# Kernel tuning notes

Hardware: AMD Instinct MI355X
Metric: run time of the kernel (lower is better)

Reference implementation:

```python
import jax, jax.numpy as jnp
import numpy as np

H = 4                      # attention heads
N_A, N_P = 20000, 30000    # author / paper node counts
E = 200000                 # edges per edge type
IN, HID, OUT = 256, 256, 128
NEG_SLOPE = 0.2


def setup_inputs() -> dict:
    key = jax.random.key(0)
    ks = jax.random.split(key, 24)

    def w(k, shape, fan_in):
        return jax.random.normal(k, shape, jnp.float32) / np.float32(np.sqrt(fan_in))

    inp = {
        'x_author': jax.random.normal(ks[0], (N_A, IN), jnp.float32),
        'x_paper':  jax.random.normal(ks[1], (N_P, IN), jnp.float32),
        'src_ap': jax.random.randint(ks[2], (E,), 0, N_A, jnp.int32),
        'dst_ap': jax.random.randint(ks[3], (E,), 0, N_P, jnp.int32),
        'src_pa': jax.random.randint(ks[4], (E,), 0, N_P, jnp.int32),
        'dst_pa': jax.random.randint(ks[5], (E,), 0, N_A, jnp.int32),
        'src_pp': jax.random.randint(ks[6], (E,), 0, N_P, jnp.int32),
        'dst_pp': jax.random.randint(ks[7], (E,), 0, N_P, jnp.int32),
        'src_aa': jax.random.randint(ks[8], (E,), 0, N_A, jnp.int32),
        'dst_aa': jax.random.randint(ks[9], (E,), 0, N_A, jnp.int32),
        # layer 1 params
        'W1_a': w(ks[10], (IN, HID), IN), 'b1_a': jnp.zeros((HID,), jnp.float32),
        'W1_p': w(ks[11], (IN, HID), IN), 'b1_p': jnp.zeros((HID,), jnp.float32),
        'att1_src': w(ks[12], (4, H, HID // H), HID // H),
        'att1_dst': w(ks[13], (4, H, HID // H), HID // H),
        'q1': w(ks[14], (HID,), HID),
        'k1_W': w(ks[15], (HID, HID), HID), 'k1_b': jnp.zeros((HID,), jnp.float32),
        # layer 2 params
        'W2_a': w(ks[16], (HID, OUT), HID), 'b2_a': jnp.zeros((OUT,), jnp.float32),
        'W2_p': w(ks[17], (HID, OUT), HID), 'b2_p': jnp.zeros((OUT,), jnp.float32),
        'att2_src': w(ks[18], (4, H, OUT // H), OUT // H),
        'att2_dst': w(ks[19], (4, H, OUT // H), OUT // H),
        'q2': w(ks[20], (OUT,), OUT),
        'k2_W': w(ks[21], (OUT, OUT), OUT), 'k2_b': jnp.zeros((OUT,), jnp.float32),
    }
    return inp


def _han_layer(h, edges, att_src, att_dst, q, kW, kb, sizes):
    """One HANConv layer. h: dict node_type -> [N, H, D]."""
    outs = {nt: [] for nt in h}
    for i, (st, dt, row, col) in enumerate(edges):
        xs, xd = h[st], h[dt]
        nd = sizes[dt]
        # per-edge additive attention logits  [E, H]
        a = jax.nn.leaky_relu((xs * att_src[i]).sum(-1)[row]
                              + (xd * att_dst[i]).sum(-1)[col], NEG_SLOPE)
        # softmax over incoming edges of each dst node (segment softmax)
        amax = jax.ops.segment_max(a, col, num_segments=nd)
        ea = jnp.exp(a - amax[col])
        denom = jax.ops.segment_sum(ea, col, num_segments=nd)
        alpha = ea / (denom[col] + 1e-16)
        # weighted scatter-sum of source features  [Nd, H, D]
        agg = jax.ops.segment_sum(xs[row] * alpha[:, :, None], col, num_segments=nd)
        outs[dt].append(jax.nn.relu(agg.reshape(nd, -1)))
    # semantic (metapath-level) attention: PyG group()
    res = {}
    for nt, lst in outs.items():
        stk = jnp.stack(lst)  # [M, N, F]
        score = (q * jnp.tanh(stk @ kW + kb).mean(axis=1)).sum(-1)  # [M]
        attn = jax.nn.softmax(score, axis=0)
        res[nt] = jnp.einsum('m,mnf->nf', attn, stk)
    return res


def reference(x_author, x_paper, src_ap, dst_ap, src_pa, dst_pa, src_pp, dst_pp,
              src_aa, dst_aa, W1_a, b1_a, W1_p, b1_p, att1_src, att1_dst, q1,
              k1_W, k1_b, W2_a, b2_a, W2_p, b2_p, att2_src, att2_dst, q2,
              k2_W, k2_b):
    sizes = {'author': N_A, 'paper': N_P}
    edges = [('author', 'paper', src_ap, dst_ap),
             ('paper', 'author', src_pa, dst_pa),
             ('paper', 'paper', src_pp, dst_pp),
             ('author', 'author', src_aa, dst_aa)]
    d1 = W1_a.shape[1] // H
    h1 = {'author': (x_author @ W1_a + b1_a).reshape(N_A, H, d1),
          'paper':  (x_paper @ W1_p + b1_p).reshape(N_P, H, d1)}
    x1 = _han_layer(h1, edges, att1_src, att1_dst, q1, k1_W, k1_b, sizes)
    d2 = W2_a.shape[1] // H
    h2 = {'author': (x1['author'] @ W2_a + b2_a).reshape(N_A, H, d2),
          'paper':  (x1['paper'] @ W2_p + b2_p).reshape(N_P, H, d2)}
    x2 = _han_layer(h2, edges, att2_src, att2_dst, q2, k2_W, k2_b, sizes)
    return x2['author']
```

## Files before the change

### kernel.cpp

```cpp
#include <hip/hip_runtime.h>
#include <math.h>


#define NA 20000
#define NP 30000
#define NE 200000
#define D1 256
#define D2 128

typedef __attribute__((ext_vector_type(8))) short short8v;
typedef __attribute__((ext_vector_type(4))) float floatx4;
typedef __attribute__((ext_vector_type(8))) unsigned short ushort8v;
typedef __attribute__((ext_vector_type(4))) unsigned short ushort4v;

static __device__ __forceinline__ float lrelu(float x) { return x >= 0.f ? x : 0.2f * x; }

static __device__ __forceinline__ unsigned short bftrunc(float x) {
    return (unsigned short)(__float_as_uint(x) >> 16);
}
static __device__ __forceinline__ float bf2f(unsigned short b) {
    return __uint_as_float(((unsigned)b) << 16);
}
static __device__ __forceinline__ unsigned short bfrn(float x) {
    unsigned u = __float_as_uint(x);
    return (unsigned short)((u + 0x7FFFu + ((u >> 16) & 1u)) >> 16);
}

typedef __attribute__((address_space(1))) const unsigned int as1_uint;
typedef __attribute__((address_space(3))) unsigned int as3_uint;
static __device__ __forceinline__ void gl_lds16(const void* g, void* l) {
    __builtin_amdgcn_global_load_lds((as1_uint*)g, (as3_uint*)l, 16, 0, 0);
}

static inline int cdiv(int a, int b) { return (a + b - 1) / b; }

struct CsrBatch {
    const int* srcv[4];
    const int* dstv[4];
    int* cnt[4];
    int* csrc[4];
    int* cdst[4];
};

__global__ __launch_bounds__(256) void count_deg_b(CsrBatch c, int n) {
    const int ty = blockIdx.y;
    const int i = blockIdx.x * 256 + threadIdx.x;
    if (i < n) atomicAdd(&c.cnt[ty][c.dstv[ty][i]], 1);
}

__global__ __launch_bounds__(256) void fill_csr_b(CsrBatch c, int n) {
    const int ty = blockIdx.y;
    const int i = blockIdx.x * 256 + threadIdx.x;
    if (i < n) {
        const int d = c.dstv[ty][i];
        const int p = atomicAdd(&c.cnt[ty][d], 1);
        c.csrc[ty][p] = c.srcv[ty][i];
        c.cdst[ty][p] = d;
    }
}

__global__ __launch_bounds__(1024) void exscan4(int* __restrict__ curbase,
                                                int* __restrict__ rpbase) {
    const int off_c[4] = {0, NP, NP + NA, NP + NA + NP};
    const int off_r[4] = {0, NP + 1, NP + NA + 2, NP + NA + NP + 3};
    const int ns[4] = {NP, NA, NP, NA};
    const int b = blockIdx.x;
    int* cur = curbase + off_c[b];
    int* rp = rpbase + off_r[b];
    const int n = ns[b];
    __shared__ int wsum[16];
    __shared__ int carry_s;
    const int t = threadIdx.x, wv = t >> 6, ln = t & 63;
    if (t == 0) carry_s = 0;
    __syncthreads();
    for (int base = 0; base < n; base += 1024) {
        const int i = base + t;
        const int v = (i < n) ? cur[i] : 0;
        int x = v;
#pragma unroll
        for (int off = 1; off < 64; off <<= 1) {
            int y = __shfl_up(x, off);
            if (ln >= off) x += y;
        }
        if (ln == 63) wsum[wv] = x;
        __syncthreads();
        if (wv == 0) {
            int s = (ln < 16) ? wsum[ln] : 0;
#pragma unroll
            for (int off = 1; off < 16; off <<= 1) {
                int y = __shfl_up(s, off);
                if (ln >= off) s += y;
            }
            if (ln < 16) wsum[ln] = s;
        }
        __syncthreads();
        const int woff = (wv == 0) ? 0 : wsum[wv - 1];
        const int c = carry_s;
        const int ex = c + woff + x - v;
        if (i < n) { rp[i] = ex; cur[i] = ex; }
        __syncthreads();
        if (t == 1023) carry_s = c + wsum[15];
        __syncthreads();
    }
    if (t == 0) rp[n] = carry_s;
}

struct PrepBatch {
    const float* W[6];
    unsigned short* img[6];
    int N[6];
    int nsl[6];
};

__global__ __launch_bounds__(256) void w_prep(PrepBatch p) {
    const int m = blockIdx.y;
    const int idx = blockIdx.x * 256 + threadIdx.x;
    if (idx >= p.nsl[m]) return;
    const int N = p.N[m];
    const int slot = idx & 3;
    const int col = (idx >> 2) % N;
    const int rest = (idx >> 2) / N;
    const int part = rest & 1;
    const int kt = rest >> 1;
    const int ks = slot ^ ((col >> 1) & 3);
    unsigned short* dst = p.img[m] + (((size_t)(kt * 2 + part) * N + col) * 32) + slot * 8;
    const float* wsrc = p.W[m] + (size_t)(kt * 32 + ks * 8) * N + col;
    short8v o;
#pragma unroll
    for (int k = 0; k < 8; ++k) {
        const float x = wsrc[(size_t)k * N];
        const unsigned short hb = bftrunc(x);
        o[k] = part ? (short)bftrunc(x - bf2f(hb)) : (short)hb;
    }
    *(short8v*)dst = o;
}

struct XrBatch {
    const float* x[2];
    unsigned short* o[2];
    int n8[2];
};

__global__ __launch_bounds__(256) void xround_b(XrBatch p) {
    const int m = blockIdx.y;
    const int i = blockIdx.x * 256 + threadIdx.x;
    if (i >= p.n8[m]) return;
    const float* xp = p.x[m] + (size_t)i * 8;
    float4 v0 = *(const float4*)xp;
    float4 v1 = *(const float4*)(xp + 4);
    const float xs8[8] = {v0.x, v0.y, v0.z, v0.w, v1.x, v1.y, v1.z, v1.w};
    short8v o;
#pragma unroll
    for (int k = 0; k < 8; ++k) o[k] = (short)bfrn(xs8[k]);
    *(short8v*)&p.o[m][(size_t)i * 8] = o;
}

template <int NT>
struct GemmBatch {
    const unsigned short* A[NT];
    const unsigned short* Wimg[NT];
    const float* bias[NT];
    unsigned short* C[NT];
    int M[NT];
};

template <int BN, bool SCORE, bool SPLITW, int NT>
__global__ __launch_bounds__(256) void gemm_sw(
    GemmBatch<NT> g, const float* __restrict__ qv, float* __restrict__ score, int K) {
    constexpr int WGN = BN / 64;
    constexpr int WGM = 4 / WGN;
    constexpr int BM = WGM * 64;
    constexpr int NB = SPLITW ? 2 : 1;
    constexpr int ACH = BM * 32 * 2 / 1024;
    constexpr int BCH = NB * BN * 32 * 2 / 1024;
    constexpr int CPW = (ACH + BCH) / 4;
    constexpr int ASZ = BM * 64;
    constexpr int BSZ = NB * BN * 64;
    const int ty = blockIdx.y;
    const int M = g.M[ty];
    const int bm = blockIdx.x * BM;
    if (bm >= M) return;
    const unsigned short* __restrict__ A = g.A[ty];
    const unsigned short* __restrict__ Wi = g.Wimg[ty];
    const float* __restrict__ bias = g.bias[ty];
    __shared__ __attribute__((aligned(16))) unsigned short As[2][BM][32];
    __shared__ __attribute__((aligned(16))) unsigned short Bs[2][NB][BN][32];
    __shared__ float red[256];
    const int t = threadIdx.x;
    const int lane = t & 63, wid = t >> 6;
    const int wr = wid / WGN, wc = wid % WGN;
    const int fq = lane >> 4, fr = lane & 15;
    const int asl = (fq ^ ((fr >> 1) & 3)) * 16;
    const int lr = lane >> 2;
    const int lks = (lane & 3) ^ ((lane >> 3) & 3);
    floatx4 acc[4][4];
#pragma unroll
    for (int i = 0; i < 4; ++i)
#pragma unroll
        for (int j = 0; j < 4; ++j) acc[i][j] = {0.f, 0.f, 0.f, 0.f};

    const int NK = K >> 5;
    auto STAGE = [&](int b, int ki) {
        const char* wbase = (const char*)Wi + (size_t)ki * (2 * BN * 64);
#pragma unroll
        for (int ci = 0; ci < CPW; ++ci) {
            const int c = wid * CPW + ci;
            if (c < ACH) {
                const int row = c * 16 + lr;
                const char* srcp = (const char*)(A + (size_t)(bm + row) * K + ki * 32 + lks * 8);
                gl_lds16(srcp, (char*)As + b * ASZ + c * 1024);
            } else {
                const int bc = c - ACH;
                gl_lds16(wbase + (size_t)bc * 1024 + lane * 16, (char*)Bs + b * BSZ + bc * 1024);
            }
        }
    };
    STAGE(0, 0);
    __syncthreads();
    int cur = 0;
    for (int ki = 0; ki < NK; ++ki) {
        if (ki + 1 < NK) STAGE(cur ^ 1, ki + 1);
        short8v a[4], bh[4], bl[4];
#pragma unroll
        for (int f = 0; f < 4; ++f) {
            const int ar = wr * 64 + f * 16 + fr;
            a[f] = *(const short8v*)((const char*)As + cur * ASZ + ar * 64 + asl);
            const int bc = wc * 64 + f * 16 + fr;
            bh[f] = *(const short8v*)((const char*)Bs + cur * BSZ + bc * 64 + asl);
            if constexpr (SPLITW)
                bl[f] = *(const short8v*)((const char*)Bs + cur * BSZ + (size_t)BN * 64 + bc * 64 + asl);
        }
#pragma unroll
        for (int i = 0; i < 4; ++i)
#pragma unroll
            for (int j = 0; j < 4; ++j) {
                acc[i][j] = __builtin_amdgcn_mfma_f32_16x16x32_bf16(a[i], bh[j], acc[i][j], 0, 0, 0);
                if constexpr (SPLITW)
                    acc[i][j] = __builtin_amdgcn_mfma_f32_16x16x32_bf16(a[i], bl[j], acc[i][j], 0, 0, 0);
            }
        __syncthreads();
        cur ^= 1;
    }
    if constexpr (!SCORE) {
        unsigned short* __restrict__ Cb = g.C[ty];
#pragma unroll
        for (int i = 0; i < 4; ++i) {
            const int gr0 = bm + wr * 64 + i * 16 + fq * 4;
#pragma unroll
            for (int j = 0; j < 4; ++j) {
                const int col = wc * 64 + j * 16 + fr;
                const float b = bias[col];
#pragma unroll
                for (int r = 0; r < 4; ++r) {
                    const int gr = gr0 + r;
                    if (gr < M) Cb[(size_t)gr * BN + col] = bfrn(acc[i][j][r] + b);
                }
            }
        }
    } else {
        float partial = 0.f;
#pragma unroll
        for (int i = 0; i < 4; ++i) {
            const int gr0 = bm + wr * 64 + i * 16 + fq * 4;
#pragma unroll
            for (int j = 0; j < 4; ++j) {
                const int col = wc * 64 + j * 16 + fr;
                const float b = bias[col], q = qv[col];
#pragma unroll
                for (int r = 0; r < 4; ++r) {
                    if (gr0 + r < M) partial += tanhf(acc[i][j][r] + b) * q;
                }
            }
        }
        red[t] = partial;
        __syncthreads();
        for (int s = 128; s > 0; s >>= 1) {
            if (t < s) red[t] += red[t + s];
            __syncthreads();
        }
        if (t == 0) atomicAdd(&score[ty], red[0]);
    }
}

template <int HD, int NSC>
__global__ __launch_bounds__(256) void node_scoresN(
    const unsigned short* __restrict__ hx,
    const float* __restrict__ a0, const float* __restrict__ a1,
    const float* __restrict__ a2, const float* __restrict__ a3,
    float* __restrict__ o0, float* __restrict__ o1,
    float* __restrict__ o2, float* __restrict__ o3, int n) {
    const int idx = blockIdx.x * blockDim.x + threadIdx.x;
    const int node = idx >> 2, hh = idx & 3;
    if (node >= n) return;
    const unsigned short* row = hx + (size_t)node * (4 * HD) + hh * HD;
    float s0 = 0.f, s1 = 0.f, s2 = 0.f, s3 = 0.f;
#pragma unroll
    for (int d = 0; d < HD; d += 4) {
        ushort4v xv = *(const ushort4v*)&row[d];
        const float x0 = bf2f(xv[0]), x1 = bf2f(xv[1]), x2 = bf2f(xv[2]), x3 = bf2f(xv[3]);
        float4 v = *(const float4*)&a0[hh * HD + d];
        s0 += x0 * v.x + x1 * v.y + x2 * v.z + x3 * v.w;
        if constexpr (NSC > 1) {
            v = *(const float4*)&a1[hh * HD + d];
            s1 += x0 * v.x + x1 * v.y + x2 * v.z + x3 * v.w;
        }
        if constexpr (NSC > 2) {
            v = *(const float4*)&a2[hh * HD + d];
            s2 += x0 * v.x + x1 * v.y + x2 * v.z + x3 * v.w;
        }
        if constexpr (NSC > 3) {
            v = *(const float4*)&a3[hh * HD + d];
            s3 += x0 * v.x + x1 * v.y + x2 * v.z + x3 * v.w;
        }
    }
    o0[idx] = s0;
    if constexpr (NSC > 1) o1[idx] = s1;
    if constexpr (NSC > 2) o2[idx] = s2;
    if constexpr (NSC > 3) o3[idx] = s3;
}

template <int NT>
struct ElogBatch {
    const int* csrc[NT];
    const int* cdst[NT];
    const float* ss[NT];
    const float* sd[NT];
    float4* alog[NT];
};

template <int NT>
__global__ __launch_bounds__(256) void edge_logits_b(ElogBatch<NT> a, int n) {
    const int ty = blockIdx.y;
    const int i = blockIdx.x * 256 + threadIdx.x;
    if (i >= n) return;
    const int s = a.csrc[ty][i], d = a.cdst[ty][i];
    const float4 av = *(const float4*)&a.ss[ty][s * 4];
    const float4 bv = *(const float4*)&a.sd[ty][d * 4];
    float4 o = {lrelu(av.x + bv.x), lrelu(av.y + bv.y), lrelu(av.z + bv.z), lrelu(av.w + bv.w)};
    a.alog[ty][i] = o;
}

template <int EPL>
static __device__ __forceinline__ void accum(const unsigned short* p, float ea, float* acc) {
#pragma unroll
    for (int w = 0; w < EPL / 8; ++w) {
        ushort8v x = *(const ushort8v*)(p + w * 8);
#pragma unroll
        for (int k = 0; k < 8; ++k) acc[w * 8 + k] += bf2f(x[k]) * ea;
    }
}

template <int NT>
struct AggBatch {
    const unsigned short* xs[NT];
    const float* alog[NT];
    const int* csrc[NT];
    const int* rowptr[NT];
    unsigned short* out[NT];
    int ndst[NT];
};

template <int D, int NT>
__global__ __launch_bounds__(256) void agg_b(AggBatch<NT> a) {
    constexpr int EPL = D / 16;
    const int ty = blockIdx.y;
    const int gid = blockIdx.x * 16 + (threadIdx.x >> 4);
    if (gid >= a.ndst[ty]) return;
    const int g = threadIdx.x & 15;
    const int h = g >> 2, sub = g & 3;
    const int* __restrict__ rp = a.rowptr[ty];
    const int e0 = rp[gid], e1 = rp[gid + 1];
    const float* __restrict__ lg = a.alog[ty];
    const int* __restrict__ cs = a.csrc[ty];
    const unsigned short* __restrict__ xs = a.xs[ty];
    float mx = -INFINITY;
    for (int e = e0 + sub; e < e1; e += 4)
        mx = fmaxf(mx, lg[(size_t)e * 4 + h]);
    mx = fmaxf(mx, __shfl_xor(mx, 1));
    mx = fmaxf(mx, __shfl_xor(mx, 2));
    float acc[EPL] = {};
    float denom = 0.f;
    int e = e0;
    for (; e + 2 <= e1; e += 2) {
        const int r0 = cs[e], r1 = cs[e + 1];
        const float l0 = lg[(size_t)e * 4 + h];
        const float l1 = lg[(size_t)(e + 1) * 4 + h];
        const float ea0 = __expf(l0 - mx), ea1 = __expf(l1 - mx);
        denom += ea0 + ea1;
        accum<EPL>(xs + (size_t)r0 * D + g * EPL, ea0, acc);
        accum<EPL>(xs + (size_t)r1 * D + g * EPL, ea1, acc);
    }
    if (e < e1) {
        const int r0 = cs[e];
        const float l0 = lg[(size_t)e * 4 + h];
        const float ea0 = __expf(l0 - mx);
        denom += ea0;
        accum<EPL>(xs + (size_t)r0 * D + g * EPL, ea0, acc);
    }
    const float inv = 1.f / (denom + 1e-16f);
    unsigned short* __restrict__ orow = a.out[ty] + (size_t)gid * D + g * EPL;
#pragma unroll
    for (int w = 0; w < EPL / 8; ++w) {
        short8v o;
#pragma unroll
        for (int k = 0; k < 8; ++k)
            o[k] = (short)bfrn(fmaxf(acc[w * 8 + k] * inv, 0.f));
        *(short8v*)&orow[w * 8] = o;
    }
}

struct CombBatch {
    const unsigned short* a[2];
    const unsigned short* b[2];
    unsigned short* o[2];
    int n8[2];
    int slot[2];
    float invN[2];
};

__global__ __launch_bounds__(256) void combine_b(CombBatch c, const float* __restrict__ sc) {
    const int ty = blockIdx.y;
    const int i = blockIdx.x * 256 + threadIdx.x;
    if (i >= c.n8[ty]) return;
    const float s0 = sc[c.slot[ty]] * c.invN[ty];
    const float s1 = sc[c.slot[ty] + 1] * c.invN[ty];
    const float m = fmaxf(s0, s1);
    const float e0 = expf(s0 - m), e1 = expf(s1 - m);
    const float w0 = e0 / (e0 + e1), w1 = e1 / (e0 + e1);
    const size_t o = (size_t)i * 8;
    ushort8v x = *(const ushort8v*)&c.a[ty][o];
    ushort8v y = *(const ushort8v*)&c.b[ty][o];
    short8v r;
#pragma unroll
    for (int k = 0; k < 8; ++k)
        r[k] = (short)bfrn(w0 * bf2f(x[k]) + w1 * bf2f(y[k]));
    *(short8v*)&c.o[ty][o] = r;
}

__global__ __launch_bounds__(256) void combine_out(
    const unsigned short* __restrict__ a, const unsigned short* __restrict__ b,
    float* __restrict__ out, const float* __restrict__ sc, int slot, float invN, int n8) {
    const int i = blockIdx.x * 256 + threadIdx.x;
    if (i >= n8) return;
    const float s0 = sc[slot] * invN, s1 = sc[slot + 1] * invN;
    const float m = fmaxf(s0, s1);
    const float e0 = expf(s0 - m), e1 = expf(s1 - m);
    const float w0 = e0 / (e0 + e1), w1 = e1 / (e0 + e1);
    const size_t o = (size_t)i * 8;
    ushort8v x = *(const ushort8v*)&a[o];
    ushort8v y = *(const ushort8v*)&b[o];
    float rr[8];
#pragma unroll
    for (int k = 0; k < 8; ++k) rr[k] = w0 * bf2f(x[k]) + w1 * bf2f(y[k]);
    float4 r0 = {rr[0], rr[1], rr[2], rr[3]};
    float4 r1 = {rr[4], rr[5], rr[6], rr[7]};
    *(float4*)&out[o] = r0;
    *(float4*)&out[o + 4] = r1;
}

extern "C" void kernel_launch(void* const* d_in, const int* in_sizes, int n_in,
                              void* d_out, int out_size, void* d_ws, size_t ws_size,
                              hipStream_t stream) {
    const float* x_a = (const float*)d_in[0];
    const float* x_p = (const float*)d_in[1];
    const int* src[4] = {(const int*)d_in[2], (const int*)d_in[4], (const int*)d_in[6], (const int*)d_in[8]};
    const int* dst[4] = {(const int*)d_in[3], (const int*)d_in[5], (const int*)d_in[7], (const int*)d_in[9]};
    const float* W1a = (const float*)d_in[10]; const float* b1a = (const float*)d_in[11];
    const float* W1p = (const float*)d_in[12]; const float* b1p = (const float*)d_in[13];
    const float* att1s = (const float*)d_in[14]; const float* att1d = (const float*)d_in[15];
    const float* q1 = (const float*)d_in[16];
    const float* k1W = (const float*)d_in[17]; const float* k1b = (const float*)d_in[18];
    const float* W2a = (const float*)d_in[19]; const float* b2a = (const float*)d_in[20];
    const float* W2p = (const float*)d_in[21]; const float* b2p = (const float*)d_in[22];
    const float* att2s = (const float*)d_in[23]; const float* att2d = (const float*)d_in[24];
    const float* q2 = (const float*)d_in[25];
    const float* k2W = (const float*)d_in[26]; const float* k2b = (const float*)d_in[27];

    const int NAp = NA + 128, NPp = NP + 128;
    char* wp = (char*)d_ws;
    unsigned short* xa_bf = (unsigned short*)wp; wp += (size_t)NAp * D1 * 2;
    unsigned short* xp_bf = (unsigned short*)wp; wp += (size_t)NPp * D1 * 2;
    unsigned short* h1a_bf = (unsigned short*)wp; wp += (size_t)NA * D1 * 2;
    unsigned short* h1p_bf = (unsigned short*)wp; wp += (size_t)NP * D1 * 2;
    unsigned short* a0 = (unsigned short*)wp; wp += (size_t)NPp * D1 * 2;
    unsigned short* a1 = (unsigned short*)wp; wp += (size_t)NAp * D1 * 2;
    unsigned short* a2 = (unsigned short*)wp; wp += (size_t)NPp * D1 * 2;
    unsigned short* a3 = (unsigned short*)wp; wp += (size_t)NAp * D1 * 2;
    float* sv = (float*)wp; wp += (size_t)(16 * NA + 16 * NP) * 4;
    float4* alogb = (float4*)wp; wp += (size_t)4 * NE * 16;
    float* sc = (float*)wp; wp += 16 * 4;
    int* rp_base = (int*)wp; wp += (size_t)(NP + NA + NP + NA + 4) * 4;
    int* cur_base = (int*)wp; wp += (size_t)(NP + NA + NP + NA) * 4;
    int* csrc_base = (int*)wp; wp += (size_t)4 * NE * 4;
    int* cdst_base = (int*)wp; wp += (size_t)4 * NE * 4;
    unsigned short* img_w1a = (unsigned short*)wp; wp += (size_t)8 * 2 * 256 * 32 * 2;
    unsigned short* img_w1p = (unsigned short*)wp; wp += (size_t)8 * 2 * 256 * 32 * 2;
    unsigned short* img_k1w = (unsigned short*)wp; wp += (size_t)8 * 2 * 256 * 32 * 2;
    unsigned short* img_w2a = (unsigned short*)wp; wp += (size_t)8 * 2 * 128 * 32 * 2;
    unsigned short* img_w2p = (unsigned short*)wp; wp += (size_t)8 * 2 * 128 * 32 * 2;
    unsigned short* img_k2w = (unsigned short*)wp; wp += (size_t)4 * 2 * 128 * 32 * 2;
    const size_t need_bytes = (size_t)(wp - (char*)d_ws);
    if (ws_size < need_bytes) return;

    int* rp[4] = {rp_base, rp_base + NP + 1, rp_base + NP + NA + 2, rp_base + NP + NA + NP + 3};
    int* cur[4] = {cur_base, cur_base + NP, cur_base + NP + NA, cur_base + NP + NA + NP};
    int* csrc[4]; int* cdst[4]; float4* alog[4];
    for (int i = 0; i < 4; ++i) {
        csrc[i] = csrc_base + (size_t)i * NE;
        cdst[i] = cdst_base + (size_t)i * NE;
        alog[i] = alogb + (size_t)i * NE;
    }
    float* ss0 = sv;             float* sd0 = ss0 + NA * 4;
    float* ss1 = sd0 + NP * 4;   float* sd1 = ss1 + NP * 4;
    float* ss2 = sd1 + NA * 4;   float* sd2 = ss2 + NP * 4;
    float* ss3 = sd2 + NP * 4;   float* sd3 = ss3 + NA * 4;
    unsigned short* res_p = a0;
    unsigned short* res_a = a1;
    unsigned short* h2a_bf = a2;
    unsigned short* h2p_bf = a2 + (size_t)NA * D2;
    unsigned short* g21 = a3;
    unsigned short* g23 = a3 + (size_t)NAp * D2;
    float* ss21 = sv;             float* sd21 = ss21 + NP * 4;
    float* ss23 = sd21 + NA * 4;  float* sd23 = ss23 + NA * 4;

    hipMemsetAsync(cur_base, 0, (size_t)(NP + NA + NP + NA) * sizeof(int), stream);
    hipMemsetAsync(sc, 0, 16 * sizeof(float), stream);
    PrepBatch pb = {{W1a, W1p, k1W, W2a, W2p, k2W},
                    {img_w1a, img_w1p, img_k1w, img_w2a, img_w2p, img_k2w},
                    {256, 256, 256, 128, 128, 128},
                    {8 * 2 * 256 * 4, 8 * 2 * 256 * 4, 8 * 2 * 256 * 4,
                     8 * 2 * 128 * 4, 8 * 2 * 128 * 4, 4 * 2 * 128 * 4}};
    w_prep<<<dim3(cdiv(8 * 2 * 256 * 4, 256), 6), 256, 0, stream>>>(pb);
    XrBatch xb = {{x_a, x_p}, {xa_bf, xp_bf}, {NA * D1 / 8, NP * D1 / 8}};
    xround_b<<<dim3(cdiv(NP * D1 / 8, 256), 2), 256, 0, stream>>>(xb);

    CsrBatch cb;
    for (int i = 0; i < 4; ++i) {
        cb.srcv[i] = src[i]; cb.dstv[i] = dst[i];
        cb.cnt[i] = cur[i]; cb.csrc[i] = csrc[i]; cb.cdst[i] = cdst[i];
    }
    count_deg_b<<<dim3(cdiv(NE, 256), 4), 256, 0, stream>>>(cb, NE);
    exscan4<<<4, 1024, 0, stream>>>(cur_base, rp_base);
    fill_csr_b<<<dim3(cdiv(NE, 256), 4), 256, 0, stream>>>(cb, NE);

    GemmBatch<2> t1 = {{xa_bf, xp_bf}, {img_w1a, img_w1p}, {b1a, b1p}, {h1a_bf, h1p_bf}, {NA, NP}};
    gemm_sw<256, false, true, 2><<<dim3(cdiv(NP, 64), 2), 256, 0, stream>>>(t1, nullptr, nullptr, 256);

    node_scoresN<64, 4><<<cdiv(NA * 4, 256), 256, 0, stream>>>(
        h1a_bf, att1s + 0 * 256, att1d + 1 * 256, att1s + 3 * 256, att1d + 3 * 256,
        ss0, sd1, ss3, sd3, NA);
    node_scoresN<64, 4><<<cdiv(NP * 4, 256), 256, 0, stream>>>(
        h1p_bf, att1d + 0 * 256, att1s + 1 * 256, att1s + 2 * 256, att1d + 2 * 256,
        sd0, ss1, ss2, sd2, NP);

    ElogBatch<4> el1 = {{csrc[0], csrc[1], csrc[2], csrc[3]},
                        {cdst[0], cdst[1], cdst[2], cdst[3]},
                        {ss0, ss1, ss2, ss3}, {sd0, sd1, sd2, sd3},
                        {alog[0], alog[1], alog[2], alog[3]}};
    edge_logits_b<4><<<dim3(cdiv(NE, 256), 4), 256, 0, stream>>>(el1, NE);
    AggBatch<4> ab1 = {{h1a_bf, h1p_bf, h1p_bf, h1a_bf},
                       {(const float*)alog[0], (const float*)alog[1], (const float*)alog[2], (const float*)alog[3]},
                       {csrc[0], csrc[1], csrc[2], csrc[3]},
                       {rp[0], rp[1], rp[2], rp[3]},
                       {a0, a1, a2, a3},
                       {NP, NA, NP, NA}};
    agg_b<256, 4><<<dim3(cdiv(NP, 16), 4), 256, 0, stream>>>(ab1);

    GemmBatch<4> s1 = {{a0, a2, a1, a3},
                       {img_k1w, img_k1w, img_k1w, img_k1w},
                       {k1b, k1b, k1b, k1b},
                       {nullptr, nullptr, nullptr, nullptr},
                       {NP, NP, NA, NA}};
    gemm_sw<256, true, false, 4><<<dim3(cdiv(NP, 64), 4), 256, 0, stream>>>(s1, q1, sc, 256);
    CombBatch c1 = {{a0, a1}, {a2, a3}, {res_p, res_a},
                    {NP * D1 / 8, NA * D1 / 8}, {0, 2}, {1.f / NP, 1.f / NA}};
    combine_b<<<dim3(cdiv(NP * D1 / 8, 256), 2), 256, 0, stream>>>(c1, sc);

    GemmBatch<2> t2 = {{res_a, res_p}, {img_w2a, img_w2p}, {b2a, b2p}, {h2a_bf, h2p_bf}, {NA, NP}};
    gemm_sw<128, false, true, 2><<<dim3(cdiv(NP, 128), 2), 256, 0, stream>>>(t2, nullptr, nullptr, 256);

    node_scoresN<32, 3><<<cdiv(NA * 4, 256), 256, 0, stream>>>(
        h2a_bf, att2d + 1 * 128, att2s + 3 * 128, att2d + 3 * 128, nullptr,
        sd21, ss23, sd23, nullptr, NA);
    node_scoresN<32, 1><<<cdiv(NP * 4, 256), 256, 0, stream>>>(
        h2p_bf, att2s + 1 * 128, nullptr, nullptr, nullptr,
        ss21, nullptr, nullptr, nullptr, NP);
    ElogBatch<2> el2 = {{csrc[1], csrc[3]}, {cdst[1], cdst[3]},
                        {ss21, ss23}, {sd21, sd23}, {alog[1], alog[3]}};
    edge_logits_b<2><<<dim3(cdiv(NE, 256), 2), 256, 0, stream>>>(el2, NE);
    AggBatch<2> ab2 = {{h2p_bf, h2a_bf},
                       {(const float*)alog[1], (const float*)alog[3]},
                       {csrc[1], csrc[3]}, {rp[1], rp[3]},
                       {g21, g23}, {NA, NA}};
    agg_b<128, 2><<<dim3(cdiv(NA, 16), 2), 256, 0, stream>>>(ab2);

    GemmBatch<2> s2 = {{g21, g23}, {img_k2w, img_k2w}, {k2b, k2b}, {nullptr, nullptr}, {NA, NA}};
    gemm_sw<128, true, false, 2><<<dim3(cdiv(NA, 128), 2), 256, 0, stream>>>(s2, q2, sc + 4, 128);
    combine_out<<<cdiv(NA * D2 / 8, 256), 256, 0, stream>>>(
        g21, g23, (float*)d_out, sc, 4, 1.f / NA, NA * D2 / 8);
}
```

Measured before the change: 417.0 us.

## Fuse edge logits into aggregation, batch node-score kernels, retile GEMM to 128 rows

Edge-logit materialisation is removed: the aggregation kernel now computes leaky-ReLU logits from the per-node source and destination scores directly, and it drops the max-subtraction pass. The two node-score launches per layer become one batched launch, and the two memsets are merged into one. The GEMM is retiled to a fixed 128-row block on a 2x2 wave grid, loading B fragments inside the j loop to cut register pressure. Dropping the softmax max-shift risks overflow in exp for large logits, and the retile changes per-block work and occupancy.

```diff
diff --git a/kernel.cpp b/kernel.cpp
--- a/kernel.cpp
+++ b/kernel.cpp
@@ -167,12 +167,13 @@
 template <int BN, bool SCORE, bool SPLITW, int NT>
 __global__ __launch_bounds__(256) void gemm_sw(
     GemmBatch<NT> g, const float* __restrict__ qv, float* __restrict__ score, int K) {
-    constexpr int WGN = BN / 64;
-    constexpr int WGM = 4 / WGN;
-    constexpr int BM = WGM * 64;
+    constexpr int BM = 128;
+    constexpr int WGM = 2, WGN = 2;
+    constexpr int CW = BN / WGN;
+    constexpr int FB = CW / 16;
     constexpr int NB = SPLITW ? 2 : 1;
-    constexpr int ACH = BM * 32 * 2 / 1024;
-    constexpr int BCH = NB * BN * 32 * 2 / 1024;
+    constexpr int ACH = BM * 64 / 1024;
+    constexpr int BCH = NB * BN * 64 / 1024;
     constexpr int CPW = (ACH + BCH) / 4;
     constexpr int ASZ = BM * 64;
     constexpr int BSZ = NB * BN * 64;
@@ -185,7 +186,6 @@
     const float* __restrict__ bias = g.bias[ty];
     __shared__ __attribute__((aligned(16))) unsigned short As[2][BM][32];
     __shared__ __attribute__((aligned(16))) unsigned short Bs[2][NB][BN][32];
-    __shared__ float red[256];
     const int t = threadIdx.x;
     const int lane = t & 63, wid = t >> 6;
     const int wr = wid / WGN, wc = wid % WGN;
@@ -193,11 +193,11 @@
     const int asl = (fq ^ ((fr >> 1) & 3)) * 16;
     const int lr = lane >> 2;
     const int lks = (lane & 3) ^ ((lane >> 3) & 3);
-    floatx4 acc[4][4];
+    floatx4 acc[4][FB];
 #pragma unroll
     for (int i = 0; i < 4; ++i)
 #pragma unroll
-        for (int j = 0; j < 4; ++j) acc[i][j] = {0.f, 0.f, 0.f, 0.f};
+        for (int j = 0; j < FB; ++j) acc[i][j] = {0.f, 0.f, 0.f, 0.f};
 
     const int NK = K >> 5;
     auto STAGE = [&](int b, int ki) {
@@ -220,24 +220,26 @@
     int cur = 0;
     for (int ki = 0; ki < NK; ++ki) {
         if (ki + 1 < NK) STAGE(cur ^ 1, ki + 1);
-        short8v a[4], bh[4], bl[4];
+        short8v afr[4];
 #pragma unroll
         for (int f = 0; f < 4; ++f) {
             const int ar = wr * 64 + f * 16 + fr;
-            a[f] = *(const short8v*)((const char*)As + cur * ASZ + ar * 64 + asl);
-            const int bc = wc * 64 + f * 16 + fr;
-            bh[f] = *(const short8v*)((const char*)Bs + cur * BSZ + bc * 64 + asl);
-            if constexpr (SPLITW)
-                bl[f] = *(const short8v*)((const char*)Bs + cur * BSZ + (size_t)BN * 64 + bc * 64 + asl);
-        }
-#pragma unroll
-        for (int i = 0; i < 4; ++i)
-#pragma unroll
-            for (int j = 0; j < 4; ++j) {
-                acc[i][j] = __builtin_amdgcn_mfma_f32_16x16x32_bf16(a[i], bh[j], acc[i][j], 0, 0, 0);
-                if constexpr (SPLITW)
-                    acc[i][j] = __builtin_amdgcn_mfma_f32_16x16x32_bf16(a[i], bl[j], acc[i][j], 0, 0, 0);
+            afr[f] = *(const short8v*)((const char*)As + cur * ASZ + ar * 64 + asl);
+        }
+#pragma unroll
+        for (int j = 0; j < FB; ++j) {
+            const int bc = wc * CW + j * 16 + fr;
+            short8v bh = *(const short8v*)((const char*)Bs + cur * BSZ + bc * 64 + asl);
+#pragma unroll
+            for (int i = 0; i < 4; ++i)
+                acc[i][j] = __builtin_amdgcn_mfma_f32_16x16x32_bf16(afr[i], bh, acc[i][j], 0, 0, 0);
+            if constexpr (SPLITW) {
+                short8v bl = *(const short8v*)((const char*)Bs + cur * BSZ + (size_t)BN * 64 + bc * 64 + asl);
+#pragma unroll
+                for (int i = 0; i < 4; ++i)
+                    acc[i][j] = __builtin_amdgcn_mfma_f32_16x16x32_bf16(afr[i], bl, acc[i][j], 0, 0, 0);
             }
+        }
         __syncthreads();
         cur ^= 1;
     }
@@ -247,8 +249,8 @@
         for (int i = 0; i < 4; ++i) {
             const int gr0 = bm + wr * 64 + i * 16 + fq * 4;
 #pragma unroll
-            for (int j = 0; j < 4; ++j) {
-                const int col = wc * 64 + j * 16 + fr;
+            for (int j = 0; j < FB; ++j) {
+                const int col = wc * CW + j * 16 + fr;
                 const float b = bias[col];
 #pragma unroll
                 for (int r = 0; r < 4; ++r) {
@@ -258,13 +260,14 @@
             }
         }
     } else {
+        __shared__ float red[256];
         float partial = 0.f;
 #pragma unroll
         for (int i = 0; i < 4; ++i) {
             const int gr0 = bm + wr * 64 + i * 16 + fq * 4;
 #pragma unroll
-            for (int j = 0; j < 4; ++j) {
-                const int col = wc * 64 + j * 16 + fr;
+            for (int j = 0; j < FB; ++j) {
+                const int col = wc * CW + j * 16 + fr;
                 const float b = bias[col], q = qv[col];
 #pragma unroll
                 for (int r = 0; r < 4; ++r) {
@@ -282,62 +285,38 @@
     }
 }
 
-template <int HD, int NSC>
-__global__ __launch_bounds__(256) void node_scoresN(
-    const unsigned short* __restrict__ hx,
-    const float* __restrict__ a0, const float* __restrict__ a1,
-    const float* __restrict__ a2, const float* __restrict__ a3,
-    float* __restrict__ o0, float* __restrict__ o1,
-    float* __restrict__ o2, float* __restrict__ o3, int n) {
-    const int idx = blockIdx.x * blockDim.x + threadIdx.x;
+struct NsBatch {
+    const unsigned short* hx[2];
+    const float* att[2][4];
+    float* out[2][4];
+    int n[2];
+    int nsc[2];
+};
+
+template <int HD>
+__global__ __launch_bounds__(256) void ns_b(NsBatch p) {
+    const int ty = blockIdx.y;
+    const int idx = blockIdx.x * 256 + threadIdx.x;
     const int node = idx >> 2, hh = idx & 3;
-    if (node >= n) return;
-    const unsigned short* row = hx + (size_t)node * (4 * HD) + hh * HD;
-    float s0 = 0.f, s1 = 0.f, s2 = 0.f, s3 = 0.f;
+    if (node >= p.n[ty]) return;
+    const unsigned short* row = p.hx[ty] + (size_t)node * (4 * HD) + hh * HD;
+    const int nsc = p.nsc[ty];
+    float s[4] = {0.f, 0.f, 0.f, 0.f};
 #pragma unroll
     for (int d = 0; d < HD; d += 4) {
         ushort4v xv = *(const ushort4v*)&row[d];
         const float x0 = bf2f(xv[0]), x1 = bf2f(xv[1]), x2 = bf2f(xv[2]), x3 = bf2f(xv[3]);
-        float4 v = *(const float4*)&a0[hh * HD + d];
-        s0 += x0 * v.x + x1 * v.y + x2 * v.z + x3 * v.w;
-        if constexpr (NSC > 1) {
-            v = *(const float4*)&a1[hh * HD + d];
-            s1 += x0 * v.x + x1 * v.y + x2 * v.z + x3 * v.w;
-        }
-        if constexpr (NSC > 2) {
-            v = *(const float4*)&a2[hh * HD + d];
-            s2 += x0 * v.x + x1 * v.y + x2 * v.z + x3 * v.w;
-        }
-        if constexpr (NSC > 3) {
-            v = *(const float4*)&a3[hh * HD + d];
-            s3 += x0 * v.x + x1 * v.y + x2 * v.z + x3 * v.w;
-        }
-    }
-    o0[idx] = s0;
-    if constexpr (NSC > 1) o1[idx] = s1;
-    if constexpr (NSC > 2) o2[idx] = s2;
-    if constexpr (NSC > 3) o3[idx] = s3;
-}
-
-template <int NT>
-struct ElogBatch {
-    const int* csrc[NT];
-    const int* cdst[NT];
-    const float* ss[NT];
-    const float* sd[NT];
-    float4* alog[NT];
-};
-
-template <int NT>
-__global__ __launch_bounds__(256) void edge_logits_b(ElogBatch<NT> a, int n) {
-    const int ty = blockIdx.y;
-    const int i = blockIdx.x * 256 + threadIdx.x;
-    if (i >= n) return;
-    const int s = a.csrc[ty][i], d = a.cdst[ty][i];
-    const float4 av = *(const float4*)&a.ss[ty][s * 4];
-    const float4 bv = *(const float4*)&a.sd[ty][d * 4];
-    float4 o = {lrelu(av.x + bv.x), lrelu(av.y + bv.y), lrelu(av.z + bv.z), lrelu(av.w + bv.w)};
-    a.alog[ty][i] = o;
+#pragma unroll
+        for (int v = 0; v < 4; ++v) {
+            if (v < nsc) {
+                float4 a = *(const float4*)&p.att[ty][v][hh * HD + d];
+                s[v] += x0 * a.x + x1 * a.y + x2 * a.z + x3 * a.w;
+            }
+        }
+    }
+#pragma unroll
+    for (int v = 0; v < 4; ++v)
+        if (v < nsc) p.out[ty][v][idx] = s[v];
 }
 
 template <int EPL>
@@ -353,7 +332,8 @@
 template <int NT>
 struct AggBatch {
     const unsigned short* xs[NT];
-    const float* alog[NT];
+    const float* ss[NT];
+    const float* sd[NT];
     const int* csrc[NT];
     const int* rowptr[NT];
     unsigned short* out[NT];
@@ -367,33 +347,29 @@
     const int gid = blockIdx.x * 16 + (threadIdx.x >> 4);
     if (gid >= a.ndst[ty]) return;
     const int g = threadIdx.x & 15;
-    const int h = g >> 2, sub = g & 3;
+    const int h = g >> 2;
     const int* __restrict__ rp = a.rowptr[ty];
     const int e0 = rp[gid], e1 = rp[gid + 1];
-    const float* __restrict__ lg = a.alog[ty];
+    const float* __restrict__ ss = a.ss[ty];
     const int* __restrict__ cs = a.csrc[ty];
     const unsigned short* __restrict__ xs = a.xs[ty];
-    float mx = -INFINITY;
-    for (int e = e0 + sub; e < e1; e += 4)
-        mx = fmaxf(mx, lg[(size_t)e * 4 + h]);
-    mx = fmaxf(mx, __shfl_xor(mx, 1));
-    mx = fmaxf(mx, __shfl_xor(mx, 2));
+    const float sdh = a.sd[ty][gid * 4 + h];
     float acc[EPL] = {};
     float denom = 0.f;
     int e = e0;
     for (; e + 2 <= e1; e += 2) {
         const int r0 = cs[e], r1 = cs[e + 1];
-        const float l0 = lg[(size_t)e * 4 + h];
-        const float l1 = lg[(size_t)(e + 1) * 4 + h];
-        const float ea0 = __expf(l0 - mx), ea1 = __expf(l1 - mx);
+        const float l0 = lrelu(ss[r0 * 4 + h] + sdh);
+        const float l1 = lrelu(ss[r1 * 4 + h] + sdh);
+        const float ea0 = __expf(l0), ea1 = __expf(l1);
         denom += ea0 + ea1;
         accum<EPL>(xs + (size_t)r0 * D + g * EPL, ea0, acc);
         accum<EPL>(xs + (size_t)r1 * D + g * EPL, ea1, acc);
     }
     if (e < e1) {
         const int r0 = cs[e];
-        const float l0 = lg[(size_t)e * 4 + h];
-        const float ea0 = __expf(l0 - mx);
+        const float l0 = lrelu(ss[r0 * 4 + h] + sdh);
+        const float ea0 = __expf(l0);
         denom += ea0;
         accum<EPL>(xs + (size_t)r0 * D + g * EPL, ea0, acc);
     }
@@ -487,10 +463,9 @@
     unsigned short* a2 = (unsigned short*)wp; wp += (size_t)NPp * D1 * 2;
     unsigned short* a3 = (unsigned short*)wp; wp += (size_t)NAp * D1 * 2;
     float* sv = (float*)wp; wp += (size_t)(16 * NA + 16 * NP) * 4;
-    float4* alogb = (float4*)wp; wp += (size_t)4 * NE * 16;
-    float* sc = (float*)wp; wp += 16 * 4;
     int* rp_base = (int*)wp; wp += (size_t)(NP + NA + NP + NA + 4) * 4;
     int* cur_base = (int*)wp; wp += (size_t)(NP + NA + NP + NA) * 4;
+    float* sc = (float*)wp; wp += 16 * 4;
     int* csrc_base = (int*)wp; wp += (size_t)4 * NE * 4;
     int* cdst_base = (int*)wp; wp += (size_t)4 * NE * 4;
     unsigned short* img_w1a = (unsigned short*)wp; wp += (size_t)8 * 2 * 256 * 32 * 2;
@@ -504,11 +479,10 @@
 
     int* rp[4] = {rp_base, rp_base + NP + 1, rp_base + NP + NA + 2, rp_base + NP + NA + NP + 3};
     int* cur[4] = {cur_base, cur_base + NP, cur_base + NP + NA, cur_base + NP + NA + NP};
-    int* csrc[4]; int* cdst[4]; float4* alog[4];
+    int* csrc[4]; int* cdst[4];
     for (int i = 0; i < 4; ++i) {
         csrc[i] = csrc_base + (size_t)i * NE;
         cdst[i] = cdst_base + (size_t)i * NE;
-        alog[i] = alogb + (size_t)i * NE;
     }
     float* ss0 = sv;             float* sd0 = ss0 + NA * 4;
     float* ss1 = sd0 + NP * 4;   float* sd1 = ss1 + NP * 4;
@@ -523,8 +497,7 @@
     float* ss21 = sv;             float* sd21 = ss21 + NP * 4;
     float* ss23 = sd21 + NA * 4;  float* sd23 = ss23 + NA * 4;
 
-    hipMemsetAsync(cur_base, 0, (size_t)(NP + NA + NP + NA) * sizeof(int), stream);
-    hipMemsetAsync(sc, 0, 16 * sizeof(float), stream);
+    hipMemsetAsync(cur_base, 0, (size_t)(NP + NA + NP + NA) * sizeof(int) + 16 * sizeof(float), stream);
     PrepBatch pb = {{W1a, W1p, k1W, W2a, W2p, k2W},
                     {img_w1a, img_w1p, img_k1w, img_w2a, img_w2p, img_k2w},
                     {256, 256, 256, 128, 128, 128},
@@ -544,22 +517,21 @@
     fill_csr_b<<<dim3(cdiv(NE, 256), 4), 256, 0, stream>>>(cb, NE);
 
     GemmBatch<2> t1 = {{xa_bf, xp_bf}, {img_w1a, img_w1p}, {b1a, b1p}, {h1a_bf, h1p_bf}, {NA, NP}};
-    gemm_sw<256, false, true, 2><<<dim3(cdiv(NP, 64), 2), 256, 0, stream>>>(t1, nullptr, nullptr, 256);
-
-    node_scoresN<64, 4><<<cdiv(NA * 4, 256), 256, 0, stream>>>(
-        h1a_bf, att1s + 0 * 256, att1d + 1 * 256, att1s + 3 * 256, att1d + 3 * 256,
-        ss0, sd1, ss3, sd3, NA);
-    node_scoresN<64, 4><<<cdiv(NP * 4, 256), 256, 0, stream>>>(
-        h1p_bf, att1d + 0 * 256, att1s + 1 * 256, att1s + 2 * 256, att1d + 2 * 256,
-        sd0, ss1, ss2, sd2, NP);
-
-    ElogBatch<4> el1 = {{csrc[0], csrc[1], csrc[2], csrc[3]},
-                        {cdst[0], cdst[1], cdst[2], cdst[3]},
-                        {ss0, ss1, ss2, ss3}, {sd0, sd1, sd2, sd3},
-                        {alog[0], alog[1], alog[2], alog[3]}};
-    edge_logits_b<4><<<dim3(cdiv(NE, 256), 4), 256, 0, stream>>>(el1, NE);
+    gemm_sw<256, false, true, 2><<<dim3(cdiv(NP, 128), 2), 256, 0, stream>>>(t1, nullptr, nullptr, 256);
+
+    NsBatch n1;
+    n1.hx[0] = h1a_bf; n1.hx[1] = h1p_bf;
+    n1.att[0][0] = att1s + 0 * 256; n1.att[0][1] = att1d + 1 * 256;
+    n1.att[0][2] = att1s + 3 * 256; n1.att[0][3] = att1d + 3 * 256;
+    n1.att[1][0] = att1d + 0 * 256; n1.att[1][1] = att1s + 1 * 256;
+    n1.att[1][2] = att1s + 2 * 256; n1.att[1][3] = att1d + 2 * 256;
+    n1.out[0][0] = ss0; n1.out[0][1] = sd1; n1.out[0][2] = ss3; n1.out[0][3] = sd3;
+    n1.out[1][0] = sd0; n1.out[1][1] = ss1; n1.out[1][2] = ss2; n1.out[1][3] = sd2;
+    n1.n[0] = NA; n1.n[1] = NP; n1.nsc[0] = 4; n1.nsc[1] = 4;
+    ns_b<64><<<dim3(cdiv(NP * 4, 256), 2), 256, 0, stream>>>(n1);
+
     AggBatch<4> ab1 = {{h1a_bf, h1p_bf, h1p_bf, h1a_bf},
-                       {(const float*)alog[0], (const float*)alog[1], (const float*)alog[2], (const float*)alog[3]},
+                       {ss0, ss1, ss2, ss3}, {sd0, sd1, sd2, sd3},
                        {csrc[0], csrc[1], csrc[2], csrc[3]},
                        {rp[0], rp[1], rp[2], rp[3]},
                        {a0, a1, a2, a3},
@@ -571,7 +543,7 @@
                        {k1b, k1b, k1b, k1b},
                        {nullptr, nullptr, nullptr, nullptr},
                        {NP, NP, NA, NA}};
-    gemm_sw<256, true, false, 4><<<dim3(cdiv(NP, 64), 4), 256, 0, stream>>>(s1, q1, sc, 256);
+    gemm_sw<256, true, false, 4><<<dim3(cdiv(NP, 128), 4), 256, 0, stream>>>(s1, q1, sc, 256);
     CombBatch c1 = {{a0, a1}, {a2, a3}, {res_p, res_a},
                     {NP * D1 / 8, NA * D1 / 8}, {0, 2}, {1.f / NP, 1.f / NA}};
     combine_b<<<dim3(cdiv(NP * D1 / 8, 256), 2), 256, 0, stream>>>(c1, sc);
@@ -579,17 +551,19 @@
     GemmBatch<2> t2 = {{res_a, res_p}, {img_w2a, img_w2p}, {b2a, b2p}, {h2a_bf, h2p_bf}, {NA, NP}};
     gemm_sw<128, false, true, 2><<<dim3(cdiv(NP, 128), 2), 256, 0, stream>>>(t2, nullptr, nullptr, 256);
 
-    node_scoresN<32, 3><<<cdiv(NA * 4, 256), 256, 0, stream>>>(
-        h2a_bf, att2d + 1 * 128, att2s + 3 * 128, att2d + 3 * 128, nullptr,
-        sd21, ss23, sd23, nullptr, NA);
-    node_scoresN<32, 1><<<cdiv(NP * 4, 256), 256, 0, stream>>>(
-        h2p_bf, att2s + 1 * 128, nullptr, nullptr, nullptr,
-        ss21, nullptr, nullptr, nullptr, NP);
-    ElogBatch<2> el2 = {{csrc[1], csrc[3]}, {cdst[1], cdst[3]},
-                        {ss21, ss23}, {sd21, sd23}, {alog[1], alog[3]}};
-    edge_logits_b<2><<<dim3(cdiv(NE, 256), 2), 256, 0, stream>>>(el2, NE);
+    NsBatch n2;
+    n2.hx[0] = h2a_bf; n2.hx[1] = h2p_bf;
+    n2.att[0][0] = att2d + 1 * 128; n2.att[0][1] = att2s + 3 * 128;
+    n2.att[0][2] = att2d + 3 * 128; n2.att[0][3] = nullptr;
+    n2.att[1][0] = att2s + 1 * 128; n2.att[1][1] = nullptr;
+    n2.att[1][2] = nullptr; n2.att[1][3] = nullptr;
+    n2.out[0][0] = sd21; n2.out[0][1] = ss23; n2.out[0][2] = sd23; n2.out[0][3] = nullptr;
+    n2.out[1][0] = ss21; n2.out[1][1] = nullptr; n2.out[1][2] = nullptr; n2.out[1][3] = nullptr;
+    n2.n[0] = NA; n2.n[1] = NP; n2.nsc[0] = 3; n2.nsc[1] = 1;
+    ns_b<32><<<dim3(cdiv(NP * 4, 256), 2), 256, 0, stream>>>(n2);
+
     AggBatch<2> ab2 = {{h2p_bf, h2a_bf},
-                       {(const float*)alog[1], (const float*)alog[3]},
+                       {ss21, ss23}, {sd21, sd23},
                        {csrc[1], csrc[3]}, {rp[1], rp[3]},
                        {g21, g23}, {NA, NA}};
     agg_b<128, 2><<<dim3(cdiv(NA, 16), 2), 256, 0, stream>>>(ab2);
```

Result: slower. 455.2 us (+9.2%).
